# Kernel optimization log

Measured on AMD Instinct MI355X. Metric: run time of the kernel, lower is better.

## Reference

```python
import jax, jax.numpy as jnp
import numpy as np

S = 16384   # num src nodes
D = 16384   # num dst nodes
FS = 128    # src feature len
FD = 128    # dst feature len
R = 50.0    # dist threshold (m)
L = 2005.0  # box side so avg degree ~ 32
LN_EPS = 1e-5


def setup_inputs() -> dict:
    rng = np.random.default_rng(0)
    src_pos_np = rng.uniform(0.0, L, (S, 2)).astype(np.float32)
    dst_pos_np = rng.uniform(0.0, L, (D, 2)).astype(np.float32)
    # radius-graph edge construction (data-dependent, done once outside jit)
    es, ed = [], []
    CH = 2048
    for i in range(0, S, CH):
        d = np.linalg.norm(src_pos_np[i:i + CH, None, :] - dst_pos_np[None, :, :], axis=-1)
        si, di = np.nonzero(d <= R)
        es.append((si + i).astype(np.int32))
        ed.append(di.astype(np.int32))
    edge_src_idx = jnp.asarray(np.concatenate(es))
    edge_dst_idx = jnp.asarray(np.concatenate(ed))

    key = jax.random.key(0)
    ks = jax.random.split(key, 12)
    w = lambda k, shape: (jax.random.normal(k, shape, jnp.float32) * 0.02)
    return {
        'src_node_features': jax.random.normal(ks[0], (S, FS), jnp.float32),
        'src_node_pos': jnp.asarray(src_pos_np),
        'dst_node_features': jax.random.normal(ks[1], (D, FD), jnp.float32),
        'dst_node_pos': jnp.asarray(dst_pos_np),
        'src_w': w(ks[2], (FS, FS)), 'src_b': jnp.zeros((FS,), jnp.float32),
        'dst_w': w(ks[3], (FD, FD)), 'dst_b': jnp.zeros((FD,), jnp.float32),
        'dist_w': w(ks[4], (2, FD)), 'dist_b': jnp.zeros((FD,), jnp.float32),
        'edge_w1': w(ks[5], (FS + FD + FD, FD)), 'edge_b1': jnp.zeros((FD,), jnp.float32),
        'edge_w2': w(ks[6], (FD, FD)), 'edge_b2': jnp.zeros((FD,), jnp.float32),
        'ln_g': jnp.ones((FD,), jnp.float32), 'ln_b': jnp.zeros((FD,), jnp.float32),
        'out_w': w(ks[7], (FD, FD)), 'out_b': jnp.zeros((FD,), jnp.float32),
        'edge_src_idx': edge_src_idx,
        'edge_dst_idx': edge_dst_idx,
    }


def reference(src_node_features, src_node_pos, dst_node_features, dst_node_pos,
              src_w, src_b, dst_w, dst_b, dist_w, dist_b,
              edge_w1, edge_b1, edge_w2, edge_b2, ln_g, ln_b, out_w, out_b,
              edge_src_idx, edge_dst_idx):
    # node encoders: Linear + ReLU
    src_enc = jax.nn.relu(src_node_features @ src_w + src_b)   # [S, FS]
    dst_enc = jax.nn.relu(dst_node_features @ dst_w + dst_b)   # [D, FD]
    # gather per-edge
    e_src = src_enc[edge_src_idx]                               # [E, FS]
    e_dst = dst_enc[edge_dst_idx]                               # [E, FD]
    e_dpos = src_node_pos[edge_src_idx] - dst_node_pos[edge_dst_idx]  # [E, 2]
    e_dist = jax.nn.relu(e_dpos @ dist_w + dist_b)              # [E, FD]
    # edge MLP: Linear-ReLU-Linear on concat [E, FS+FD+FD]
    e_in = jnp.concatenate([e_src, e_dist, e_dst], axis=-1)
    e_out = jax.nn.relu(e_in @ edge_w1 + edge_b1) @ edge_w2 + edge_b2  # [E, FD]
    # scatter-add to destination nodes
    agg = dst_enc + jax.ops.segment_sum(e_out, edge_dst_idx, num_segments=D)
    # LayerNorm + ReLU + Linear + residual + ReLU
    mu = jnp.mean(agg, axis=-1, keepdims=True)
    var = jnp.mean(jnp.square(agg - mu), axis=-1, keepdims=True)
    ln = (agg - mu) * jax.lax.rsqrt(var + LN_EPS) * ln_g + ln_b
    h = jax.nn.relu(ln) @ out_w + out_b + dst_node_features
    return jax.nn.relu(h)
```

## Files before the change

kernel.cpp:

```cpp
#include <hip/hip_runtime.h>

typedef unsigned short ushort_t;
typedef unsigned int uint_t;
typedef short bhalf8 __attribute__((ext_vector_type(8)));
typedef float f32x4 __attribute__((ext_vector_type(4)));
typedef float f32x2 __attribute__((ext_vector_type(2)));

#define DEG_CAP 96

__device__ __forceinline__ float b2f(ushort_t u) {
    union { uint_t i; float f; } v; v.i = ((uint_t)u) << 16; return v.f;
}
__device__ __forceinline__ float u2f(uint_t u) {
    union { uint_t i; float f; } v; v.i = u; return v.f;
}
__device__ __forceinline__ ushort_t f2b(float f) {
    union { float f; uint_t i; } v; v.f = f;
    uint_t r = v.i + 0x7fffu + ((v.i >> 16) & 1u);
    return (ushort_t)(r >> 16);
}
__device__ __forceinline__ uint_t f2u(float f) {
    union { float f; uint_t i; } v; v.f = f; return v.i;
}
__device__ __forceinline__ uint_t pack_trunc(float lo, float hi) {
    return __builtin_amdgcn_perm(f2u(hi), f2u(lo), 0x07060302u);
}
__device__ __forceinline__ uint_t pack_rhu(float lo, float hi) {
    return __builtin_amdgcn_perm(f2u(hi) + 0x8000u, f2u(lo) + 0x8000u, 0x07060302u);
}
__device__ __forceinline__ uint_t addpack_trunc(uint_t a, uint_t b) {
    float lo = u2f(a << 16) + u2f(b << 16);
    float hi = u2f(a & 0xffff0000u) + u2f(b & 0xffff0000u);
    return __builtin_amdgcn_perm(f2u(hi), f2u(lo), 0x07060302u);
}

__global__ __launch_bounds__(256) void prep_kernel(
    const float* __restrict__ wsrc, const float* __restrict__ wdst,
    const float* __restrict__ w2,   const float* __restrict__ wout,
    const float* __restrict__ w1,
    ushort_t* __restrict__ msrc, ushort_t* __restrict__ mdst,
    ushort_t* __restrict__ m2,   ushort_t* __restrict__ mout,
    ushort_t* __restrict__ m1a,  ushort_t* __restrict__ m1b,
    ushort_t* __restrict__ m1c,
    const int* __restrict__ esi, const int* __restrict__ edi, int E,
    int* __restrict__ deg, int* __restrict__ bucket,
    int4* __restrict__ edge_sd, int EpadI,
    int countB, int zeroB)
{
    int b = blockIdx.x, tid = threadIdx.x;
    if (b < 56) {
        const float* ins[7] = { wsrc, wdst, w2, wout, w1, w1 + 16384, w1 + 32768 };
        ushort_t* outs[7]   = { msrc, mdst, m2, mout, m1a, m1b, m1c };
        int mat = b >> 3;
        const float* in = ins[mat];
        ushort_t* out = outs[mat];
        int flat = (b & 7)*256 + tid;
        int nt = flat >> 8, rem = flat & 255;
        int ks = rem >> 6, lane = rem & 63;
        int q = lane >> 4, m = lane & 15;
        #pragma unroll
        for (int j = 0; j < 8; ++j)
            out[flat*8 + j] = f2b(in[(ks*32 + q*8 + j)*128 + nt*16 + m]);
    } else if (b < 56 + countB) {
        int i = (b - 56)*256 + tid;
        if (i < E) {
            int d = edi[i];
            int p = atomicAdd(&deg[d], 1);
            if (p < DEG_CAP) bucket[(size_t)d*DEG_CAP + p] = esi[i];
        }
    } else {
        int zb = b - 56 - countB;
        for (int i = zb*256 + tid; i < EpadI; i += zeroB*256)
            edge_sd[i] = make_int4(0, -1, 0, 0);
    }
}

__global__ __launch_bounds__(256) void enc2_kernel(
    const float* __restrict__ src_feat, const float* __restrict__ dst_feat,
    const ushort_t* __restrict__ msrc, const ushort_t* __restrict__ mdst,
    const ushort_t* __restrict__ m1a,  const ushort_t* __restrict__ m1c,
    const float* __restrict__ src_b,   const float* __restrict__ dst_b,
    const float* __restrict__ b1,
    ushort_t* __restrict__ Csrc, ushort_t* __restrict__ Cdst,
    ushort_t* __restrict__ dst_enc,
    const int* __restrict__ deg, int* __restrict__ P,
    int Dn, int Sb, int Db)
{
    int tid = threadIdx.x, blk = blockIdx.x;

    if (blk == Sb + Db) {
        __shared__ int sums[256];
        int per = Dn >> 8;
        const int4* d4 = (const int4*)(deg + tid*per);
        int4 v[16]; int s = 0;
        #pragma unroll
        for (int k = 0; k < 16; ++k) {
            v[k] = d4[k];
            v[k].x = min(v[k].x, DEG_CAP); v[k].y = min(v[k].y, DEG_CAP);
            v[k].z = min(v[k].z, DEG_CAP); v[k].w = min(v[k].w, DEG_CAP);
            s += v[k].x + v[k].y + v[k].z + v[k].w;
        }
        sums[tid] = s;
        __syncthreads();
        for (int off = 1; off < 256; off <<= 1) {
            int x = (tid >= off) ? sums[tid - off] : 0;
            __syncthreads();
            sums[tid] += x;
            __syncthreads();
        }
        int run = sums[tid] - s;
        int4* n4 = (int4*)(P + tid*per);
        #pragma unroll
        for (int k = 0; k < 16; ++k) {
            int4 o;
            o.x = run; run += v[k].x;
            o.y = run; run += v[k].y;
            o.z = run; run += v[k].z;
            o.w = run; run += v[k].w;
            n4[k] = o;
        }
        if (tid == 255) P[Dn] = run;
        return;
    }

    __shared__ ushort_t A_l[64*136];
    __shared__ ushort_t E_l[64*136];
    __shared__ float b_l[128];
    __shared__ float b2_l[128];

    const float* A; const ushort_t *W1m, *W2m; const float* bias; const float* bias2;
    ushort_t *outC, *outEnc; int rowbase;
    if (blk < Sb) { A = src_feat; W1m = msrc; W2m = m1a; bias = src_b;
                    outC = Csrc; outEnc = nullptr; rowbase = blk*64; bias2 = nullptr; }
    else          { A = dst_feat; W1m = mdst; W2m = m1c; bias = dst_b;
                    outC = Cdst; outEnc = dst_enc; rowbase = (blk - Sb)*64; bias2 = b1; }

    const float4* A4 = (const float4*)A;
    for (int i = tid; i < 2048; i += 256) {
        int r = i >> 5, c = i & 31;
        float4 v = A4[(size_t)(rowbase + r)*32 + c];
        uint2 u;
        u.x = pack_trunc(v.x, v.y);
        u.y = pack_trunc(v.z, v.w);
        *(uint2*)(A_l + r*136 + c*4) = u;
    }
    if (tid < 128) { b_l[tid] = bias[tid]; b2_l[tid] = bias2 ? bias2[tid] : 0.f; }
    __syncthreads();

    int lane = tid & 63, w = tid >> 6, q = lane >> 4, m = lane & 15;
    const bhalf8* Wv1 = (const bhalf8*)W1m;
    f32x4 acc[4][2] = {};
    #pragma unroll
    for (int ks = 0; ks < 4; ++ks) {
        bhalf8 bf0 = Wv1[((2*w)*4 + ks)*64 + lane];
        bhalf8 bf1 = Wv1[((2*w+1)*4 + ks)*64 + lane];
        #pragma unroll
        for (int mt = 0; mt < 4; ++mt) {
            bhalf8 a = *(const bhalf8*)(A_l + (mt*16 + m)*136 + ks*32 + q*8);
            acc[mt][0] = __builtin_amdgcn_mfma_f32_16x16x32_bf16(a, bf0, acc[mt][0], 0, 0, 0);
            acc[mt][1] = __builtin_amdgcn_mfma_f32_16x16x32_bf16(a, bf1, acc[mt][1], 0, 0, 0);
        }
    }
    #pragma unroll
    for (int mt = 0; mt < 4; ++mt)
    #pragma unroll
    for (int nt = 0; nt < 2; ++nt)
    #pragma unroll
    for (int reg = 0; reg < 4; ++reg) {
        int col = w*32 + nt*16 + m;
        int row = mt*16 + q*4 + reg;
        E_l[row*136 + col] = f2b(fmaxf(acc[mt][nt][reg] + b_l[col], 0.f));
    }
    __syncthreads();

    if (outEnc) {
        for (int i = tid; i < 1024; i += 256) {
            int r = i >> 4, c = i & 15;
            ((uint4*)outEnc)[(size_t)(rowbase + r)*16 + c] = *(const uint4*)(E_l + r*136 + c*8);
        }
    }

    const bhalf8* Wv2 = (const bhalf8*)W2m;
    f32x4 acc2[4][2] = {};
    #pragma unroll
    for (int ks = 0; ks < 4; ++ks) {
        bhalf8 bf0 = Wv2[((2*w)*4 + ks)*64 + lane];
        bhalf8 bf1 = Wv2[((2*w+1)*4 + ks)*64 + lane];
        #pragma unroll
        for (int mt = 0; mt < 4; ++mt) {
            bhalf8 a = *(const bhalf8*)(E_l + (mt*16 + m)*136 + ks*32 + q*8);
            acc2[mt][0] = __builtin_amdgcn_mfma_f32_16x16x32_bf16(a, bf0, acc2[mt][0], 0, 0, 0);
            acc2[mt][1] = __builtin_amdgcn_mfma_f32_16x16x32_bf16(a, bf1, acc2[mt][1], 0, 0, 0);
        }
    }
    #pragma unroll
    for (int mt = 0; mt < 4; ++mt)
    #pragma unroll
    for (int nt = 0; nt < 2; ++nt)
    #pragma unroll
    for (int reg = 0; reg < 4; ++reg) {
        int col = w*32 + nt*16 + m;
        int row = mt*16 + q*4 + reg;
        A_l[row*136 + col] = f2b(acc2[mt][nt][reg] + b2_l[col]);
    }
    __syncthreads();
    for (int i = tid; i < 1024; i += 256) {
        int r = i >> 4, c = i & 15;
        ((uint4*)outC)[(size_t)(rowbase + r)*16 + c] = *(const uint4*)(A_l + r*136 + c*8);
    }
}

__global__ __launch_bounds__(256) void csr_kernel(
    const int* __restrict__ P, const int* __restrict__ deg,
    const int* __restrict__ bucket,
    const float* __restrict__ src_pos, const float* __restrict__ dst_pos,
    int4* __restrict__ edge_sd, int Dn)
{
    int t = blockIdx.x*256 + threadIdx.x;
    int d = t >> 2, pl = t & 3;
    if (d >= Dn) return;
    int st = P[d];
    int n = min(deg[d], DEG_CAP);
    float2 dp = ((const float2*)dst_pos)[d];
    const int* bk = bucket + (size_t)d*DEG_CAP;
    for (int p = pl; p < n; p += 4) {
        int s = bk[p];
        float2 sp = ((const float2*)src_pos)[s];
        edge_sd[st + p] = make_int4(s, d,
                                    __float_as_int(sp.x - dp.x),
                                    __float_as_int(sp.y - dp.y));
    }
}

__global__ __launch_bounds__(512, 6) void edgeagg_kernel(
    const ushort_t* __restrict__ Csrc, const ushort_t* __restrict__ Cdst,
    const int4* __restrict__ edge_sd, const int* __restrict__ P,
    const ushort_t* __restrict__ w1bm,
    const float* __restrict__ dist_w, const float* __restrict__ dist_b,
    const ushort_t* __restrict__ w2m, const float* __restrict__ b2,
    const ushort_t* __restrict__ dst_enc,
    const float* __restrict__ ln_g, const float* __restrict__ ln_b,
    const ushort_t* __restrict__ moutm, const float* __restrict__ out_b,
    const float* __restrict__ dst_feat, float* __restrict__ out)
{
    __shared__ char pool[18432];
    __shared__ char poolG[17408];
    __shared__ __align__(16) ushort_t ld16[64];
    __shared__ float2 dxy_l[64];
    __shared__ float dw0_l[128], dw1_l[128], db_l[128];

    ushort_t* X   = (ushort_t*)pool;
    ushort_t* Hb  = (ushort_t*)pool;
    ushort_t* A_l = (ushort_t*)pool;
    ushort_t* G   = (ushort_t*)poolG;
    float* pb2 = (float*)poolG;
    float* pg  = pb2 + 128;
    float* plb = pg  + 128;
    float* pob = plb + 128;
    float* ps  = pob + 128;
    float* ps2 = ps  + 128;
    float* muv = ps2 + 128;
    float* invv = muv + 16;
    int*   dgl  = (int*)(invv + 16);

    int tid = threadIdx.x, blk = blockIdx.x;
    int lane = tid & 63, w = tid >> 6, q = lane >> 4, m = lane & 15;
    int r0 = tid >> 4, c16 = tid & 15;

    int d0 = blk*16;
    int e0 = P[d0], e1 = P[d0 + 16];
    int nT = (e1 - e0 + 63) >> 6;

    const uint4* cs4 = (const uint4*)Csrc;
    const uint4* cd4 = (const uint4*)Cdst;

    if (tid < 128) {
        dw0_l[tid] = dist_w[tid];
        dw1_l[tid] = dist_w[128 + tid];
        db_l[tid]  = dist_b[tid];
    }

    int p_id = (w & 1)*16;
    int win = (w >> 1)*32;
    bhalf8 iden;
    #pragma unroll
    for (int j = 0; j < 8; ++j)
        iden[j] = (short)((q*8 + j == p_id + m) ? 0x3f80 : 0);

    int col = w*16 + m;
    f32x4 o = {};

    const bhalf8* Wv = (const bhalf8*)w1bm;

    for (int t = 0; t < nT; ++t) {
        size_t gbase = (size_t)e0 + (size_t)t*64;

        if (tid < 64) {
            int4 r = edge_sd[gbase + tid];
            dxy_l[tid] = make_float2(__int_as_float(r.z), __int_as_float(r.w));
            ld16[tid] = (ushort_t)(r.y - d0);
        }
        {
            int4 re0 = edge_sd[gbase + r0];
            int4 re1 = edge_sd[gbase + r0 + 32];
            uint4 ga0 = cs4[(size_t)re0.x*16 + c16];
            uint4 gb0 = cd4[(size_t)max(re0.y, 0)*16 + c16];
            uint4 ga1 = cs4[(size_t)re1.x*16 + c16];
            uint4 gb1 = cd4[(size_t)max(re1.y, 0)*16 + c16];
            uint4 u;
            u.x = addpack_trunc(ga0.x, gb0.x);
            u.y = addpack_trunc(ga0.y, gb0.y);
            u.z = addpack_trunc(ga0.z, gb0.z);
            u.w = addpack_trunc(ga0.w, gb0.w);
            *(uint4*)(G + r0*136 + c16*8) = u;
            u.x = addpack_trunc(ga1.x, gb1.x);
            u.y = addpack_trunc(ga1.y, gb1.y);
            u.z = addpack_trunc(ga1.z, gb1.z);
            u.w = addpack_trunc(ga1.w, gb1.w);
            *(uint4*)(G + (r0 + 32)*136 + c16*8) = u;
        }
        __syncthreads();

        {
            int j2 = lane*2;
            float w00 = dw0_l[j2], w01 = dw0_l[j2+1];
            float w10 = dw1_l[j2], w11 = dw1_l[j2+1];
            float bb0 = db_l[j2],  bb1 = db_l[j2+1];
            #pragma unroll
            for (int k = 0; k < 8; ++k) {
                int r = w + k*8;
                float2 dd = dxy_l[r];
                float v0 = fmaxf(fmaf(dd.x, w00, fmaf(dd.y, w10, bb0)), 0.f);
                float v1 = fmaxf(fmaf(dd.x, w01, fmaf(dd.y, w11, bb1)), 0.f);
                *(uint_t*)(X + r*136 + j2) = pack_trunc(v0, v1);
            }
        }
        __syncthreads();

        f32x4 acc[4];
        {
            bhalf8 wf0 = Wv[(w*4 + 0)*64 + lane];
            bhalf8 wf1 = Wv[(w*4 + 1)*64 + lane];
            bhalf8 wf2 = Wv[(w*4 + 2)*64 + lane];
            bhalf8 wf3 = Wv[(w*4 + 3)*64 + lane];
            #pragma unroll
            for (int mt = 0; mt < 4; ++mt) {
                f32x4 z = {};
                bhalf8 g = *(const bhalf8*)(G + (mt*16 + m)*136 + win + q*8);
                acc[mt] = __builtin_amdgcn_mfma_f32_16x16x32_bf16(g, iden, z, 0, 0, 0);
                bhalf8 a0 = *(const bhalf8*)(X + (mt*16 + m)*136 + 0*32 + q*8);
                acc[mt] = __builtin_amdgcn_mfma_f32_16x16x32_bf16(a0, wf0, acc[mt], 0, 0, 0);
                bhalf8 a1 = *(const bhalf8*)(X + (mt*16 + m)*136 + 1*32 + q*8);
                acc[mt] = __builtin_amdgcn_mfma_f32_16x16x32_bf16(a1, wf1, acc[mt], 0, 0, 0);
                bhalf8 a2 = *(const bhalf8*)(X + (mt*16 + m)*136 + 2*32 + q*8);
                acc[mt] = __builtin_amdgcn_mfma_f32_16x16x32_bf16(a2, wf2, acc[mt], 0, 0, 0);
                bhalf8 a3 = *(const bhalf8*)(X + (mt*16 + m)*136 + 3*32 + q*8);
                acc[mt] = __builtin_amdgcn_mfma_f32_16x16x32_bf16(a3, wf3, acc[mt], 0, 0, 0);
            }
        }
        __syncthreads();

        #pragma unroll
        for (int mt = 0; mt < 4; ++mt) {
            int row0 = mt*16 + q*4;
            uint2 u;
            u.x = pack_rhu(fmaxf(acc[mt][0], 0.f), fmaxf(acc[mt][1], 0.f));
            u.y = pack_rhu(fmaxf(acc[mt][2], 0.f), fmaxf(acc[mt][3], 0.f));
            *(uint2*)(Hb + col*72 + row0) = u;
        }
        __builtin_amdgcn_sched_barrier(0);

        {
            bhalf8 sv0 = *(const bhalf8*)(ld16 + q*8);
            bhalf8 sv1 = *(const bhalf8*)(ld16 + 32 + q*8);
            const ushort_t* hrow = Hb + col*72 + q*8;
            bhalf8 hb0 = *(const bhalf8*)(hrow);
            bhalf8 hb1 = *(const bhalf8*)(hrow + 32);
            const short onebf = (short)0x3f80;
            short tm = (short)m;
            bhalf8 a0, a1;
            #pragma unroll
            for (int j = 0; j < 8; ++j) {
                a0[j] = (sv0[j] == tm) ? onebf : (short)0;
                a1[j] = (sv1[j] == tm) ? onebf : (short)0;
            }
            o = __builtin_amdgcn_mfma_f32_16x16x32_bf16(a0, hb0, o, 0, 0, 0);
            o = __builtin_amdgcn_mfma_f32_16x16x32_bf16(a1, hb1, o, 0, 0, 0);
        }
        __syncthreads();
    }

    #pragma unroll
    for (int reg = 0; reg < 4; ++reg)
        A_l[(q*4 + reg)*136 + col] = f2b(o[reg]);
    if (tid < 128) { pb2[tid] = b2[tid]; pg[tid] = ln_g[tid];
                     plb[tid] = ln_b[tid]; pob[tid] = out_b[tid]; }
    if (tid < 16) dgl[tid] = P[d0 + tid + 1] - P[d0 + tid];
    __syncthreads();

    const bhalf8* Wv2 = (const bhalf8*)w2m;
    f32x4 ya = {};
    #pragma unroll
    for (int ks = 0; ks < 4; ++ks) {
        bhalf8 bf = Wv2[(w*4 + ks)*64 + lane];
        bhalf8 a = *(const bhalf8*)(A_l + m*136 + ks*32 + q*8);
        ya = __builtin_amdgcn_mfma_f32_16x16x32_bf16(a, bf, ya, 0, 0, 0);
    }
    float y[4];
    #pragma unroll
    for (int reg = 0; reg < 4; ++reg) {
        int rowl = q*4 + reg;
        y[reg] = ya[reg] + (float)dgl[rowl]*pb2[col]
               + b2f(dst_enc[(size_t)(d0 + rowl)*128 + col]);
    }

    float s[4], s2[4];
    #pragma unroll
    for (int reg = 0; reg < 4; ++reg) { s[reg] = y[reg]; s2[reg] = y[reg]*y[reg]; }
    #pragma unroll
    for (int off = 1; off < 16; off <<= 1) {
        #pragma unroll
        for (int reg = 0; reg < 4; ++reg) {
            s[reg]  += __shfl_xor(s[reg],  off);
            s2[reg] += __shfl_xor(s2[reg], off);
        }
    }
    if (m == 0) {
        #pragma unroll
        for (int reg = 0; reg < 4; ++reg) {
            ps[(q*4 + reg)*8 + w]  = s[reg];
            ps2[(q*4 + reg)*8 + w] = s2[reg];
        }
    }
    __syncthreads();
    if (tid < 16) {
        float su = 0.f, sq = 0.f;
        #pragma unroll
        for (int k = 0; k < 8; ++k) { su += ps[tid*8 + k]; sq += ps2[tid*8 + k]; }
        float mu = su / 128.f;
        float var = sq / 128.f - mu*mu;
        muv[tid] = mu;
        invv[tid] = 1.0f / sqrtf(var + 1e-5f);
    }
    __syncthreads();
    #pragma unroll
    for (int reg = 0; reg < 4; ++reg) {
        int rowl = q*4 + reg;
        float v = (y[reg] - muv[rowl])*invv[rowl]*pg[col] + plb[col];
        A_l[rowl*136 + col] = f2b(fmaxf(v, 0.f));
    }
    __syncthreads();

    const bhalf8* Wo = (const bhalf8*)moutm;
    f32x4 oa = {};
    #pragma unroll
    for (int ks = 0; ks < 4; ++ks) {
        bhalf8 bf = Wo[(w*4 + ks)*64 + lane];
        bhalf8 a = *(const bhalf8*)(A_l + m*136 + ks*32 + q*8);
        oa = __builtin_amdgcn_mfma_f32_16x16x32_bf16(a, bf, oa, 0, 0, 0);
    }
    #pragma unroll
    for (int reg = 0; reg < 4; ++reg) {
        size_t grow = (size_t)d0 + q*4 + reg;
        float v = oa[reg] + pob[col] + dst_feat[grow*128 + col];
        out[grow*128 + col] = fmaxf(v, 0.f);
    }
}

extern "C" void kernel_launch(void* const* d_in, const int* in_sizes, int n_in,
                              void* d_out, int out_size, void* d_ws, size_t ws_size,
                              hipStream_t stream)
{
    const float* src_feat = (const float*)d_in[0];
    const float* src_pos  = (const float*)d_in[1];
    const float* dst_feat = (const float*)d_in[2];
    const float* dst_pos  = (const float*)d_in[3];
    const float* src_w    = (const float*)d_in[4];
    const float* src_b    = (const float*)d_in[5];
    const float* dst_w    = (const float*)d_in[6];
    const float* dst_b    = (const float*)d_in[7];
    const float* dist_w   = (const float*)d_in[8];
    const float* dist_b   = (const float*)d_in[9];
    const float* w1       = (const float*)d_in[10];
    const float* b1       = (const float*)d_in[11];
    const float* w2       = (const float*)d_in[12];
    const float* b2       = (const float*)d_in[13];
    const float* ln_g     = (const float*)d_in[14];
    const float* ln_b     = (const float*)d_in[15];
    const float* out_w    = (const float*)d_in[16];
    const float* out_b    = (const float*)d_in[17];
    const int* esi        = (const int*)d_in[18];
    const int* edi        = (const int*)d_in[19];
    int E = in_sizes[18];
    int S = in_sizes[0] / 128;
    int D = in_sizes[2] / 128;
    int nTiles = (E + 63) / 64;
    int EpadI = nTiles*64 + 64;

    char* ws = (char*)d_ws;
    size_t off = 0;
    auto alloc = [&](size_t bytes) { char* p = ws + off; off += (bytes + 511) & ~(size_t)511; return p; };
    ushort_t* Csrc    = (ushort_t*)alloc((size_t)S*128*2);
    ushort_t* Cdst    = (ushort_t*)alloc((size_t)D*128*2);
    ushort_t* dst_enc = (ushort_t*)alloc((size_t)D*128*2);
    ushort_t* t_src   = (ushort_t*)alloc(128*128*2);
    ushort_t* t_dst   = (ushort_t*)alloc(128*128*2);
    ushort_t* t_w2    = (ushort_t*)alloc(128*128*2);
    ushort_t* t_out   = (ushort_t*)alloc(128*128*2);
    ushort_t* t_1a    = (ushort_t*)alloc(128*128*2);
    ushort_t* t_1b    = (ushort_t*)alloc(128*128*2);
    ushort_t* t_1c    = (ushort_t*)alloc(128*128*2);
    int*      deg     = (int*)     alloc((size_t)D*4);
    int*      P       = (int*)     alloc((size_t)(D + 1)*4);
    int*      bucket  = (int*)     alloc((size_t)D*DEG_CAP*4);
    int4*     edge_sd = (int4*)    alloc((size_t)EpadI*16);

    hipMemsetAsync(deg, 0, (size_t)D*4, stream);

    int countB = (E + 255)/256;
    int zeroB = 64;
    prep_kernel<<<56 + countB + zeroB, 256, 0, stream>>>(
        src_w, dst_w, w2, out_w, w1,
        t_src, t_dst, t_w2, t_out, t_1a, t_1b, t_1c,
        esi, edi, E, deg, bucket, edge_sd, EpadI, countB, zeroB);

    int Sb = S/64, Db = D/64;
    enc2_kernel<<<Sb + Db + 1, 256, 0, stream>>>(
        src_feat, dst_feat, t_src, t_dst, t_1a, t_1c, src_b, dst_b, b1,
        Csrc, Cdst, dst_enc, deg, P, D, Sb, Db);

    csr_kernel<<<(D*4 + 255)/256, 256, 0, stream>>>(
        P, deg, bucket, src_pos, dst_pos, edge_sd, D);

    edgeagg_kernel<<<D/16, 512, 0, stream>>>(
        Csrc, Cdst, edge_sd, P,
        t_1b, dist_w, dist_b,
        t_w2, b2, dst_enc, ln_g, ln_b,
        t_out, out_b, dst_feat, (float*)d_out);
}
```

Before: 213.3 us.

## Halve destinations per block and compact edge records to src/dst pairs

Each edge-aggregation block now handles 8 destination nodes instead of 16, so twice as many blocks are launched. This spreads the irregular per-block edge work more evenly across CUs. The per-edge record shrinks from an int4 carrying precomputed position deltas to an int2 of (src, dst). The deltas are recomputed inside the edge kernel from the position arrays, trading extra gathers there for less CSR write traffic. Half the 16-row MFMA tile is now padding, so the LayerNorm and output stages do wasted work, and the mask guards add some complexity.

```diff
diff --git a/kernel.cpp b/kernel.cpp
--- a/kernel.cpp
+++ b/kernel.cpp
@@ -7,6 +7,7 @@
 typedef float f32x2 __attribute__((ext_vector_type(2)));
 
 #define DEG_CAP 96
+#define NDST 8
 
 __device__ __forceinline__ float b2f(ushort_t u) {
     union { uint_t i; float f; } v; v.i = ((uint_t)u) << 16; return v.f;
@@ -44,7 +45,7 @@
     ushort_t* __restrict__ m1c,
     const int* __restrict__ esi, const int* __restrict__ edi, int E,
     int* __restrict__ deg, int* __restrict__ bucket,
-    int4* __restrict__ edge_sd, int EpadI,
+    int2* __restrict__ edge_rec, int EpadI,
     int countB, int zeroB)
 {
     int b = blockIdx.x, tid = threadIdx.x;
@@ -71,7 +72,7 @@
     } else {
         int zb = b - 56 - countB;
         for (int i = zb*256 + tid; i < EpadI; i += zeroB*256)
-            edge_sd[i] = make_int4(0, -1, 0, 0);
+            edge_rec[i] = make_int2(0, -1);
     }
 }
 
@@ -213,28 +214,22 @@
 __global__ __launch_bounds__(256) void csr_kernel(
     const int* __restrict__ P, const int* __restrict__ deg,
     const int* __restrict__ bucket,
-    const float* __restrict__ src_pos, const float* __restrict__ dst_pos,
-    int4* __restrict__ edge_sd, int Dn)
+    int2* __restrict__ edge_rec, int Dn)
 {
     int t = blockIdx.x*256 + threadIdx.x;
     int d = t >> 2, pl = t & 3;
     if (d >= Dn) return;
     int st = P[d];
     int n = min(deg[d], DEG_CAP);
-    float2 dp = ((const float2*)dst_pos)[d];
     const int* bk = bucket + (size_t)d*DEG_CAP;
-    for (int p = pl; p < n; p += 4) {
-        int s = bk[p];
-        float2 sp = ((const float2*)src_pos)[s];
-        edge_sd[st + p] = make_int4(s, d,
-                                    __float_as_int(sp.x - dp.x),
-                                    __float_as_int(sp.y - dp.y));
-    }
+    for (int p = pl; p < n; p += 4)
+        edge_rec[st + p] = make_int2(bk[p], d);
 }
 
 __global__ __launch_bounds__(512, 6) void edgeagg_kernel(
     const ushort_t* __restrict__ Csrc, const ushort_t* __restrict__ Cdst,
-    const int4* __restrict__ edge_sd, const int* __restrict__ P,
+    const float* __restrict__ src_pos, const float* __restrict__ dst_pos,
+    const int2* __restrict__ edge_rec, const int* __restrict__ P,
     const ushort_t* __restrict__ w1bm,
     const float* __restrict__ dist_w, const float* __restrict__ dist_b,
     const ushort_t* __restrict__ w2m, const float* __restrict__ b2,
@@ -267,8 +262,8 @@
     int lane = tid & 63, w = tid >> 6, q = lane >> 4, m = lane & 15;
     int r0 = tid >> 4, c16 = tid & 15;
 
-    int d0 = blk*16;
-    int e0 = P[d0], e1 = P[d0 + 16];
+    int d0 = blk*NDST;
+    int e0 = P[d0], e1 = P[d0 + NDST];
     int nT = (e1 - e0 + 63) >> 6;
 
     const uint4* cs4 = (const uint4*)Csrc;
@@ -296,13 +291,20 @@
         size_t gbase = (size_t)e0 + (size_t)t*64;
 
         if (tid < 64) {
-            int4 r = edge_sd[gbase + tid];
-            dxy_l[tid] = make_float2(__int_as_float(r.z), __int_as_float(r.w));
-            ld16[tid] = (ushort_t)(r.y - d0);
+            int2 sd = edge_rec[gbase + tid];
+            int s = sd.x, d = sd.y;
+            float dx = 0.f, dy = 0.f;
+            if (d >= 0) {
+                float2 sp = ((const float2*)src_pos)[s];
+                float2 dp = ((const float2*)dst_pos)[d];
+                dx = sp.x - dp.x; dy = sp.y - dp.y;
+            }
+            dxy_l[tid] = make_float2(dx, dy);
+            ld16[tid] = (ushort_t)(d - d0);
         }
         {
-            int4 re0 = edge_sd[gbase + r0];
-            int4 re1 = edge_sd[gbase + r0 + 32];
+            int2 re0 = edge_rec[gbase + r0];
+            int2 re1 = edge_rec[gbase + r0 + 32];
             uint4 ga0 = cs4[(size_t)re0.x*16 + c16];
             uint4 gb0 = cd4[(size_t)max(re0.y, 0)*16 + c16];
             uint4 ga1 = cs4[(size_t)re1.x*16 + c16];
@@ -395,7 +397,7 @@
         A_l[(q*4 + reg)*136 + col] = f2b(o[reg]);
     if (tid < 128) { pb2[tid] = b2[tid]; pg[tid] = ln_g[tid];
                      plb[tid] = ln_b[tid]; pob[tid] = out_b[tid]; }
-    if (tid < 16) dgl[tid] = P[d0 + tid + 1] - P[d0 + tid];
+    if (tid < 16) dgl[tid] = (tid < NDST) ? (P[d0 + tid + 1] - P[d0 + tid]) : 0;
     __syncthreads();
 
     const bhalf8* Wv2 = (const bhalf8*)w2m;
@@ -410,8 +412,9 @@
     #pragma unroll
     for (int reg = 0; reg < 4; ++reg) {
         int rowl = q*4 + reg;
+        size_t drow = (size_t)d0 + ((rowl < NDST) ? rowl : 0);
         y[reg] = ya[reg] + (float)dgl[rowl]*pb2[col]
-               + b2f(dst_enc[(size_t)(d0 + rowl)*128 + col]);
+               + b2f(dst_enc[drow*128 + col]);
     }
 
     float s[4], s2[4];
@@ -461,9 +464,12 @@
     }
     #pragma unroll
     for (int reg = 0; reg < 4; ++reg) {
-        size_t grow = (size_t)d0 + q*4 + reg;
-        float v = oa[reg] + pob[col] + dst_feat[grow*128 + col];
-        out[grow*128 + col] = fmaxf(v, 0.f);
+        int rowl = q*4 + reg;
+        if (rowl < NDST) {
+            size_t grow = (size_t)d0 + rowl;
+            float v = oa[reg] + pob[col] + dst_feat[grow*128 + col];
+            out[grow*128 + col] = fmaxf(v, 0.f);
+        }
     }
 }
 
@@ -494,8 +500,7 @@
     int E = in_sizes[18];
     int S = in_sizes[0] / 128;
     int D = in_sizes[2] / 128;
-    int nTiles = (E + 63) / 64;
-    int EpadI = nTiles*64 + 64;
+    int EpadI = E + 128;
 
     char* ws = (char*)d_ws;
     size_t off = 0;
@@ -513,7 +518,7 @@
     int*      deg     = (int*)     alloc((size_t)D*4);
     int*      P       = (int*)     alloc((size_t)(D + 1)*4);
     int*      bucket  = (int*)     alloc((size_t)D*DEG_CAP*4);
-    int4*     edge_sd = (int4*)    alloc((size_t)EpadI*16);
+    int2*     edge_rec= (int2*)    alloc((size_t)EpadI*8);
 
     hipMemsetAsync(deg, 0, (size_t)D*4, stream);
 
@@ -522,7 +527,7 @@
     prep_kernel<<<56 + countB + zeroB, 256, 0, stream>>>(
         src_w, dst_w, w2, out_w, w1,
         t_src, t_dst, t_w2, t_out, t_1a, t_1b, t_1c,
-        esi, edi, E, deg, bucket, edge_sd, EpadI, countB, zeroB);
+        esi, edi, E, deg, bucket, edge_rec, EpadI, countB, zeroB);
 
     int Sb = S/64, Db = D/64;
     enc2_kernel<<<Sb + Db + 1, 256, 0, stream>>>(
@@ -530,10 +535,10 @@
         Csrc, Cdst, dst_enc, deg, P, D, Sb, Db);
 
     csr_kernel<<<(D*4 + 255)/256, 256, 0, stream>>>(
-        P, deg, bucket, src_pos, dst_pos, edge_sd, D);
-
-    edgeagg_kernel<<<D/16, 512, 0, stream>>>(
-        Csrc, Cdst, edge_sd, P,
+        P, deg, bucket, edge_rec, D);
+
+    edgeagg_kernel<<<D/NDST, 512, 0, stream>>>(
+        Csrc, Cdst, src_pos, dst_pos, edge_rec, P,
         t_1b, dist_w, dist_b,
         t_w2, b2, dst_enc, ln_g, ln_b,
         t_out, out_b, dst_feat, (float*)d_out);
```

After: 214.7 us. About the same (+0.6%).
